# Kernel tuning notes

Measured on AMD Instinct MI355X. Metric: run time of the kernel, lower is better.

The kernel has to match this reference:

```python
import jax, jax.numpy as jnp
import numpy as np

N_EL, N_NB, DIM = 8192, 24, 256
CUTOFF = 5.0
F0, F1 = 32, 16
N_ENV = 8
N_FEAT = 4  # [dist, dx, dy, dz]


def setup_inputs() -> dict:
    key = jax.random.key(0)
    ks = jax.random.split(key, 24)
    d = {}
    d['elec'] = jax.random.normal(ks[0], (N_EL, DIM), jnp.float32)
    d['msg'] = jax.random.normal(ks[1], (N_EL, DIM), jnp.float32)
    # positions inside a box of half the cutoff so pairs are within range
    d['r'] = jax.random.uniform(ks[2], (N_EL, 3), jnp.float32) * (0.5 * CUTOFF)
    d['r_nb'] = jax.random.uniform(ks[3], (N_EL, N_NB, 3), jnp.float32) * (0.5 * CUTOFF)
    d['s'] = jax.random.randint(ks[4], (N_EL,), 0, 2, jnp.int32)
    d['s_nb'] = jax.random.randint(ks[5], (N_EL, N_NB), 0, 2, jnp.int32)
    d['hinit_nb'] = jax.random.normal(ks[6], (N_EL, N_NB, DIM), jnp.float32)
    # parameters
    def lecun(k, shape):
        fan_in = shape[0]
        return jax.random.normal(k, shape, jnp.float32) / np.float32(np.sqrt(fan_in))
    d['W_in'] = lecun(ks[7], (DIM, DIM)); d['b_in'] = jnp.zeros((DIM,), jnp.float32)
    d['ee_scales'] = jax.random.uniform(ks[8], (N_ENV,), jnp.float32, 0.5, CUTOFF)
    d['ee_kernel'] = lecun(ks[9], (N_FEAT, F0))
    d['ee_bias'] = 2.0 * jax.random.normal(ks[10], (F0,), jnp.float32)
    d['Wf'] = lecun(ks[11], (F0 + N_ENV, F1)); d['bf'] = jnp.zeros((F1,), jnp.float32)
    d['Wsame'] = lecun(ks[12], (F1, DIM))
    d['Wdiff'] = lecun(ks[13], (F1, DIM))
    d['W1'] = lecun(ks[14], (DIM, DIM)); d['b1'] = jnp.zeros((DIM,), jnp.float32)
    d['W2'] = lecun(ks[15], (DIM, DIM)); d['b2'] = jnp.zeros((DIM,), jnp.float32)
    d['W3'] = lecun(ks[16], (DIM, DIM)); d['b3'] = jnp.zeros((DIM,), jnp.float32)
    d['scale'] = jnp.float32(1.0)  # FixedScalingFactor (identity at init)
    return d


def _forward(elec, msg, r, r_nb, s, s_nb, hinit_nb,
             W_in, b_in, ee_scales, ee_kernel, ee_bias, Wf, bf,
             Wsame, Wdiff, W1, b1, W2, b2, W3, b3, scale):
    silu = jax.nn.silu
    elec1 = silu(elec @ W_in + b_in)                       # [N, D]
    # get_diff_features: [dist, dx, dy, dz]
    diff = r_nb - r[:, None, :]                             # [N, K, 3]
    dist = jnp.sqrt(jnp.sum(diff * diff, -1) + 1e-12)       # [N, K]
    feats = jnp.concatenate([dist[..., None], diff], -1)    # [N, K, 4]
    spin_mask = s[:, None] == s_nb                          # [N, K]
    # PairwiseFilter: MLP on diff-features + radial envelopes, smooth cutoff
    env = jnp.exp(-jnp.square(dist[..., None] / ee_scales)) # [N, K, E]
    h = silu(feats @ ee_kernel + ee_bias)                   # [N, K, F0]
    h = jnp.concatenate([h, env], -1)                       # [N, K, F0+E]
    x = dist / CUTOFF
    cut = jnp.where(dist < CUTOFF, jnp.square(1.0 - x) * (1.0 + 2.0 * x), 0.0)
    beta = (h @ Wf + bf) * cut[..., None]                   # [N, K, F1]
    gamma = jnp.where(spin_mask[..., None], beta @ Wsame, beta @ Wdiff)  # [N, K, D]
    hinit_msg = jnp.einsum('nid,nid->nd', silu(elec1[:, None] + hinit_nb), gamma)
    out = silu(elec1 @ W1 + b1 + hinit_msg)
    out = silu(out @ W2 + b2 + msg)
    out = silu(out @ W3 + b3)
    return (out + elec1) * scale


def reference(elec, msg, r, r_nb, s, s_nb, hinit_nb,
              W_in, b_in, ee_scales, ee_kernel, ee_bias, Wf, bf,
              Wsame, Wdiff, W1, b1, W2, b2, W3, b3, scale):
    return _forward(elec, msg, r, r_nb, s, s_nb, hinit_nb,
                    W_in, b_in, ee_scales, ee_kernel, ee_bias, Wf, bf,
                    Wsame, Wdiff, W1, b1, W2, b2, W3, b3, scale)
```

## Files before the change

kernel.cpp:

```cpp
#include <hip/hip_runtime.h>

#define DIM 256
#define PDIM 260
#define PD2  264
#define NNB 24
#define NEL 8192
#define ROWS 16
#define NT 512
#define CUTOFF 5.0f

typedef unsigned int u32;
typedef unsigned short u16;
typedef __attribute__((ext_vector_type(8))) short bf16x8;
typedef __attribute__((ext_vector_type(4))) float f32x4;

__device__ __forceinline__ u16 f2b(float f){
  union{float f;u32 i;}v; v.f=f;
  u32 r = v.i + 0x7fffu + ((v.i>>16)&1u);
  return (u16)(r>>16);
}
__device__ __forceinline__ float b2f(u16 u){
  union{u32 i;float f;}v; v.i = ((u32)u)<<16; return v.f;
}
__device__ __forceinline__ float fast_silu(float x){
  float e = __builtin_amdgcn_exp2f(-1.44269504088896340f * x);
  return x * __builtin_amdgcn_rcpf(1.0f + e);
}

__global__ __launch_bounds__(256)
void wprep(const float* __restrict__ W0, const float* __restrict__ W1,
           const float* __restrict__ W2, const float* __restrict__ W3,
           const float* __restrict__ Wsame, const float* __restrict__ Wdiff,
           u16* __restrict__ ws){
  if (blockIdx.x < 1024){
    const int mat = blockIdx.x >> 8;
    const int n   = blockIdx.x & 255;
    const int k   = threadIdx.x;
    const float* W = (mat==0)?W0:(mat==1)?W1:(mat==2)?W2:W3;
    ws[(mat<<16) + (n<<8) + k] = f2b(W[(k<<8) + n]);
  } else {
    const int n = threadIdx.x;
    u16* dst = ws + 4*65536 + n*32;
    #pragma unroll
    for (int kk = 0; kk < 16; kk++){
      dst[kk]    = f2b(Wsame[kk*DIM + n]);
      dst[16+kk] = f2b(Wdiff[kk*DIM + n]);
    }
  }
}

template<int MODE, int ABF16>
__device__ __forceinline__ void gemm_mfma(
    const void* A, u16* sE1b, float* sR1,
    const u16* __restrict__ Wt, const float* __restrict__ bias,
    const float* __restrict__ extraGbl, float* __restrict__ outGbl,
    float scl, int n0, int t)
{
  const int lane = t & 63;
  const int ln   = lane & 15;
  const int quad = lane >> 4;
  const int nt0  = (t >> 6) << 1;
  f32x4 acc0 = {0.f,0.f,0.f,0.f};
  f32x4 acc1 = {0.f,0.f,0.f,0.f};
  const u16* bp0 = Wt + (nt0*16 + ln)*DIM;
  const u16* bp1 = bp0 + 16*DIM;
  #pragma unroll
  for (int ks = 0; ks < 8; ks++){
    const int k0 = ks*32 + quad*8;
    bf16x8 af;
    if (ABF16){
      af = *(const bf16x8*)((const u16*)A + ln*PD2 + k0);
    } else {
      const float* arow = (const float*)A + ln*PDIM;
      float4 a01 = *(const float4*)(arow + k0);
      float4 a23 = *(const float4*)(arow + k0 + 4);
      af[0]=(short)f2b(a01.x); af[1]=(short)f2b(a01.y);
      af[2]=(short)f2b(a01.z); af[3]=(short)f2b(a01.w);
      af[4]=(short)f2b(a23.x); af[5]=(short)f2b(a23.y);
      af[6]=(short)f2b(a23.z); af[7]=(short)f2b(a23.w);
    }
    bf16x8 b0 = *(const bf16x8*)(bp0 + k0);
    bf16x8 b1 = *(const bf16x8*)(bp1 + k0);
    acc0 = __builtin_amdgcn_mfma_f32_16x16x32_bf16(af, b0, acc0, 0, 0, 0);
    acc1 = __builtin_amdgcn_mfma_f32_16x16x32_bf16(af, b1, acc1, 0, 0, 0);
  }
  if (MODE == 2) __syncthreads();
  #pragma unroll
  for (int r = 0; r < 4; r++){
    const int m = quad*4 + r;
    #pragma unroll
    for (int tt = 0; tt < 2; tt++){
      const int n = (nt0+tt)*16 + ln;
      float v = (tt ? acc1[r] : acc0[r]) + bias[n];
      if (MODE == 1) v += sR1[m*PDIM + n];
      if (MODE == 2) v += extraGbl[(size_t)(n0+m)*DIM + n];
      v = fast_silu(v);
      if (MODE == 0)      sE1b[m*PD2 + n] = f2b(v);
      else if (MODE == 3) outGbl[(size_t)(n0+m)*DIM + n] = (v + b2f(sE1b[m*PD2 + n])) * scl;
      else                sR1[m*PDIM + n] = v;
    }
  }
}

__global__ __launch_bounds__(NT, 6)
void fused_moon_kernel(
    const float* __restrict__ elec, const float* __restrict__ msg,
    const float* __restrict__ rpos, const float* __restrict__ rnb,
    const int* __restrict__ s,    const int* __restrict__ snb,
    const float* __restrict__ hinit,
    const float* __restrict__ bin,
    const float* __restrict__ eesc, const float* __restrict__ eek,
    const float* __restrict__ eeb,  const float* __restrict__ Wf,
    const float* __restrict__ bfb,
    const float* __restrict__ b1, const float* __restrict__ b2,
    const float* __restrict__ b3,
    const float* __restrict__ scalep,
    const u16* __restrict__ Wt,
    float* __restrict__ out)
{
  __shared__ float sR1[ROWS*PDIM];
  __shared__ u16   sE1b[ROWS*PD2];
  __shared__ u16   sBC[NNB*16*32];
  const int t  = threadIdx.x;
  const int n0 = blockIdx.x * ROWS;

  {
    const float4* ep = (const float4*)elec;
    #pragma unroll
    for (int h = 0; h < 2; h++){
      const int idx = t + h*NT;
      float4 v = ep[(size_t)n0*64 + idx];
      *(float4*)&sR1[(idx>>6)*PDIM + (idx&63)*4] = v;
    }
  }
  __syncthreads();

  gemm_mfma<0,0>(sR1, sE1b, sR1, Wt, bin, nullptr, nullptr, 0.f, n0, t);

  if (t < ROWS*NNB) {
    const int rr = t / NNB;
    const int k  = t - rr*NNB;
    const int n  = n0 + rr;
    const float* rp  = rpos + n*3;
    const float* rnp = rnb + (n*NNB + k)*3;
    float dx = rnp[0] - rp[0];
    float dy = rnp[1] - rp[1];
    float dz = rnp[2] - rp[2];
    float dist = sqrtf(dx*dx + dy*dy + dz*dz + 1e-12f);
    float feats[4] = {dist, dx, dy, dz};
    float h[32];
    #pragma unroll
    for (int f4 = 0; f4 < 8; f4++){
      float4 a4 = *(const float4*)&eeb[4*f4];
      float av[4] = {a4.x, a4.y, a4.z, a4.w};
      #pragma unroll
      for (int i = 0; i < 4; i++){
        float4 kv = *(const float4*)&eek[i*32 + 4*f4];
        av[0]+=feats[i]*kv.x; av[1]+=feats[i]*kv.y; av[2]+=feats[i]*kv.z; av[3]+=feats[i]*kv.w;
      }
      h[4*f4+0]=fast_silu(av[0]); h[4*f4+1]=fast_silu(av[1]);
      h[4*f4+2]=fast_silu(av[2]); h[4*f4+3]=fast_silu(av[3]);
    }
    float env[8];
    #pragma unroll
    for (int e = 0; e < 8; e++){
      float q = dist * __builtin_amdgcn_rcpf(eesc[e]);
      env[e] = __builtin_amdgcn_exp2f(-1.44269504088896340f * q * q);
    }
    float xx = dist * (1.0f/CUTOFF);
    float cut = (dist < CUTOFF) ? (1.0f-xx)*(1.0f-xx)*(1.0f+2.0f*xx) : 0.0f;
    float barr[16];
    #pragma unroll
    for (int j4 = 0; j4 < 4; j4++){
      float4 a4 = *(const float4*)&bfb[4*j4];
      float av[4] = {a4.x, a4.y, a4.z, a4.w};
      #pragma unroll
      for (int f = 0; f < 40; f++){
        float val = (f < 32) ? h[f] : env[f-32];
        float4 wv = *(const float4*)&Wf[f*16 + 4*j4];
        av[0]+=val*wv.x; av[1]+=val*wv.y; av[2]+=val*wv.z; av[3]+=val*wv.w;
      }
      barr[4*j4+0]=av[0]*cut; barr[4*j4+1]=av[1]*cut;
      barr[4*j4+2]=av[2]*cut; barr[4*j4+3]=av[3]*cut;
    }
    const int m = (s[n] == snb[n*NNB + k]);
    u16 vals[32];
    #pragma unroll
    for (int j = 0; j < 16; j++){
      u16 b = f2b(barr[j]);
      vals[j]    = m ? b : (u16)0;
      vals[16+j] = m ? (u16)0 : b;
    }
    u16* rowp = &sBC[(k*16 + rr)*32];
    #pragma unroll
    for (int c = 0; c < 4; c++){
      const int cp = c ^ ((rr>>1)&3);
      bf16x8 cv;
      #pragma unroll
      for (int j = 0; j < 8; j++) cv[j] = (short)vals[c*8 + j];
      *(bf16x8*)(rowp + cp*8) = cv;
    }
  }
  __syncthreads();

  {
    const int lane = t & 63;
    const int ln   = lane & 15;
    const int quad = lane >> 4;
    const int nt0  = (t >> 6) << 1;
    const u16* Wcat = Wt + 4*65536;
    bf16x8 bs0 = *(const bf16x8*)(Wcat + (nt0*16 + ln)*32 + quad*8);
    bf16x8 bs1 = *(const bf16x8*)(Wcat + ((nt0+1)*16 + ln)*32 + quad*8);
    float e1v[4][2], hm[4][2];
    #pragma unroll
    for (int j = 0; j < 4; j++){
      #pragma unroll
      for (int tt = 0; tt < 2; tt++){
        e1v[j][tt] = b2f(sE1b[(quad*4+j)*PD2 + (nt0+tt)*16 + ln]);
        hm[j][tt] = 0.f;
      }
    }
    const int cswz = (quad ^ ((ln>>1)&3))*8;
    const float* hb = hinit + (size_t)(n0 + quad*4)*NNB*DIM + ln;
    for (int k = 0; k < NNB; k++){
      bf16x8 af = *(const bf16x8*)(&sBC[(k*16 + ln)*32 + cswz]);
      f32x4 z = {0.f,0.f,0.f,0.f};
      f32x4 g0 = __builtin_amdgcn_mfma_f32_16x16x32_bf16(af, bs0, z, 0, 0, 0);
      f32x4 g1 = __builtin_amdgcn_mfma_f32_16x16x32_bf16(af, bs1, z, 0, 0, 0);
      #pragma unroll
      for (int j = 0; j < 4; j++){
        const float* hp = hb + ((size_t)(j*NNB + k))*DIM + nt0*16;
        float h0 = hp[0];
        float h1 = hp[16];
        hm[j][0] += fast_silu(e1v[j][0] + h0) * g0[j];
        hm[j][1] += fast_silu(e1v[j][1] + h1) * g1[j];
      }
    }
    #pragma unroll
    for (int j = 0; j < 4; j++){
      sR1[(quad*4+j)*PDIM + nt0*16 + ln]     = hm[j][0];
      sR1[(quad*4+j)*PDIM + (nt0+1)*16 + ln] = hm[j][1];
    }
  }
  __syncthreads();

  const float scl = scalep[0];

  gemm_mfma<1,1>(sE1b, sE1b, sR1, Wt + (1<<16), b1, nullptr, nullptr, 0.f, n0, t);
  __syncthreads();
  gemm_mfma<2,0>(sR1, sE1b, sR1, Wt + (2<<16), b2, msg, nullptr, 0.f, n0, t);
  __syncthreads();
  gemm_mfma<3,0>(sR1, sE1b, sR1, Wt + (3<<16), b3, nullptr, out, scl, n0, t);
}

extern "C" void kernel_launch(void* const* d_in, const int* in_sizes, int n_in,
                              void* d_out, int out_size, void* d_ws, size_t ws_size,
                              hipStream_t stream) {
  (void)in_sizes; (void)n_in; (void)ws_size; (void)out_size;
  const float* elec  = (const float*)d_in[0];
  const float* msg   = (const float*)d_in[1];
  const float* rpos  = (const float*)d_in[2];
  const float* rnb   = (const float*)d_in[3];
  const int*   s     = (const int*)d_in[4];
  const int*   snb   = (const int*)d_in[5];
  const float* hinit = (const float*)d_in[6];
  const float* Win   = (const float*)d_in[7];
  const float* bin   = (const float*)d_in[8];
  const float* eesc  = (const float*)d_in[9];
  const float* eek   = (const float*)d_in[10];
  const float* eeb   = (const float*)d_in[11];
  const float* Wf    = (const float*)d_in[12];
  const float* bfb   = (const float*)d_in[13];
  const float* Wsame = (const float*)d_in[14];
  const float* Wdiff = (const float*)d_in[15];
  const float* W1    = (const float*)d_in[16];
  const float* b1    = (const float*)d_in[17];
  const float* W2    = (const float*)d_in[18];
  const float* b2    = (const float*)d_in[19];
  const float* W3    = (const float*)d_in[20];
  const float* b3    = (const float*)d_in[21];
  const float* scl   = (const float*)d_in[22];
  float* outp        = (float*)d_out;
  u16*   wt          = (u16*)d_ws;

  wprep<<<dim3(1025), dim3(256), 0, stream>>>(Win, W1, W2, W3, Wsame, Wdiff, wt);
  fused_moon_kernel<<<dim3(NEL/ROWS), dim3(NT), 0, stream>>>(
      elec, msg, rpos, rnb, s, snb, hinit,
      bin, eesc, eek, eeb, Wf, bfb,
      b1, b2, b3, scl, wt, outp);
}
```

Measured before the change: 419.9 us.

## Vectorize hinit neighbor loads via LDS transpose of filter outputs, with prefetch

Each lane now reads four contiguous hinit floats per row with float4 loads, and the next neighbor's values are prefetched in registers. Before, each lane did scalar strided loads. The MFMA filter outputs go through a per-wave LDS buffer so the lane layout matches those loads. The spin-split beta tile is stored at half width with a separate mask array, and the mask is applied when the MFMA operand is built. This adds extra LDS traffic, wave barriers and shared memory, and lowers the launch-bounds occupancy hint from 6 to 4.

Result: faster. 370.5 us (-11.8%).

```diff
diff --git a/kernel.cpp b/kernel.cpp
--- a/kernel.cpp
+++ b/kernel.cpp
@@ -3,6 +3,8 @@
 #define DIM 256
 #define PDIM 260
 #define PD2  264
+#define SBPITCH 20
+#define SGPITCH 40
 #define NNB 24
 #define NEL 8192
 #define ROWS 16
@@ -102,7 +104,7 @@
   }
 }
 
-__global__ __launch_bounds__(NT, 6)
+__global__ __launch_bounds__(NT, 4)
 void fused_moon_kernel(
     const float* __restrict__ elec, const float* __restrict__ msg,
     const float* __restrict__ rpos, const float* __restrict__ rnb,
@@ -120,7 +122,9 @@
 {
   __shared__ float sR1[ROWS*PDIM];
   __shared__ u16   sE1b[ROWS*PD2];
-  __shared__ u16   sBC[NNB*16*32];
+  __shared__ u16   sBC[NNB*16*SBPITCH];
+  __shared__ int   sMask[ROWS*NNB];
+  __shared__ float sG[8*16*SGPITCH];
   const int t  = threadIdx.x;
   const int n0 = blockIdx.x * ROWS;
 
@@ -169,7 +173,7 @@
     }
     float xx = dist * (1.0f/CUTOFF);
     float cut = (dist < CUTOFF) ? (1.0f-xx)*(1.0f-xx)*(1.0f+2.0f*xx) : 0.0f;
-    float barr[16];
+    u16* rowp = &sBC[(k*16 + rr)*SBPITCH];
     #pragma unroll
     for (int j4 = 0; j4 < 4; j4++){
       float4 a4 = *(const float4*)&bfb[4*j4];
@@ -180,26 +184,12 @@
         float4 wv = *(const float4*)&Wf[f*16 + 4*j4];
         av[0]+=val*wv.x; av[1]+=val*wv.y; av[2]+=val*wv.z; av[3]+=val*wv.w;
       }
-      barr[4*j4+0]=av[0]*cut; barr[4*j4+1]=av[1]*cut;
-      barr[4*j4+2]=av[2]*cut; barr[4*j4+3]=av[3]*cut;
-    }
-    const int m = (s[n] == snb[n*NNB + k]);
-    u16 vals[32];
-    #pragma unroll
-    for (int j = 0; j < 16; j++){
-      u16 b = f2b(barr[j]);
-      vals[j]    = m ? b : (u16)0;
-      vals[16+j] = m ? (u16)0 : b;
-    }
-    u16* rowp = &sBC[(k*16 + rr)*32];
-    #pragma unroll
-    for (int c = 0; c < 4; c++){
-      const int cp = c ^ ((rr>>1)&3);
-      bf16x8 cv;
-      #pragma unroll
-      for (int j = 0; j < 8; j++) cv[j] = (short)vals[c*8 + j];
-      *(bf16x8*)(rowp + cp*8) = cv;
-    }
+      ushort4 bv;
+      bv.x = f2b(av[0]*cut); bv.y = f2b(av[1]*cut);
+      bv.z = f2b(av[2]*cut); bv.w = f2b(av[3]*cut);
+      *(ushort4*)(rowp + 4*j4) = bv;
+    }
+    sMask[rr*NNB + k] = (s[n] == snb[n*NNB + k]) ? 1 : 0;
   }
   __syncthreads();
 
@@ -207,40 +197,60 @@
     const int lane = t & 63;
     const int ln   = lane & 15;
     const int quad = lane >> 4;
-    const int nt0  = (t >> 6) << 1;
+    const int w    = t >> 6;
+    const int C0   = w << 5;
     const u16* Wcat = Wt + 4*65536;
-    bf16x8 bs0 = *(const bf16x8*)(Wcat + (nt0*16 + ln)*32 + quad*8);
-    bf16x8 bs1 = *(const bf16x8*)(Wcat + ((nt0+1)*16 + ln)*32 + quad*8);
-    float e1v[4][2], hm[4][2];
-    #pragma unroll
-    for (int j = 0; j < 4; j++){
+    bf16x8 bs0 = *(const bf16x8*)(Wcat + (C0 + ln)*32 + quad*8);
+    bf16x8 bs1 = *(const bf16x8*)(Wcat + (C0 + 16 + ln)*32 + quad*8);
+    float* sGw = &sG[w*16*SGPITCH];
+
+    const int rowA = lane >> 3;
+    const int rowB = rowA + 8;
+    const int c4   = (lane & 7) << 2;
+    float e1A[4], e1B[4];
+    {
+      ushort4 ea = *(const ushort4*)&sE1b[rowA*PD2 + C0 + c4];
+      ushort4 eb = *(const ushort4*)&sE1b[rowB*PD2 + C0 + c4];
+      e1A[0]=b2f(ea.x); e1A[1]=b2f(ea.y); e1A[2]=b2f(ea.z); e1A[3]=b2f(ea.w);
+      e1B[0]=b2f(eb.x); e1B[1]=b2f(eb.y); e1B[2]=b2f(eb.z); e1B[3]=b2f(eb.w);
+    }
+    const float* hpA = hinit + (size_t)(n0 + rowA)*NNB*DIM + C0 + c4;
+    const float* hpB = hpA + (size_t)8*NNB*DIM;
+    float hmA[4] = {0.f,0.f,0.f,0.f};
+    float hmB[4] = {0.f,0.f,0.f,0.f};
+    float4 hA = *(const float4*)(hpA);
+    float4 hB = *(const float4*)(hpB);
+    for (int k = 0; k < NNB; k++){
+      const int kn = (k+1 < NNB) ? (k+1) : (NNB-1);
+      float4 hA2 = *(const float4*)(hpA + kn*DIM);
+      float4 hB2 = *(const float4*)(hpB + kn*DIM);
+      bf16x8 b8 = *(const bf16x8*)(&sBC[(k*16 + ln)*SBPITCH + (quad&1)*8]);
+      const int mm = sMask[ln*NNB + k];
+      const u16 km = (u16)((((quad>>1) ^ mm) != 0) ? 0xFFFFu : 0u);
+      bf16x8 af;
       #pragma unroll
-      for (int tt = 0; tt < 2; tt++){
-        e1v[j][tt] = b2f(sE1b[(quad*4+j)*PD2 + (nt0+tt)*16 + ln]);
-        hm[j][tt] = 0.f;
-      }
-    }
-    const int cswz = (quad ^ ((ln>>1)&3))*8;
-    const float* hb = hinit + (size_t)(n0 + quad*4)*NNB*DIM + ln;
-    for (int k = 0; k < NNB; k++){
-      bf16x8 af = *(const bf16x8*)(&sBC[(k*16 + ln)*32 + cswz]);
+      for (int j = 0; j < 8; j++) af[j] = (short)(((u16)af[j], (u16)b8[j]) & km);
       f32x4 z = {0.f,0.f,0.f,0.f};
       f32x4 g0 = __builtin_amdgcn_mfma_f32_16x16x32_bf16(af, bs0, z, 0, 0, 0);
       f32x4 g1 = __builtin_amdgcn_mfma_f32_16x16x32_bf16(af, bs1, z, 0, 0, 0);
+      __builtin_amdgcn_wave_barrier();
       #pragma unroll
-      for (int j = 0; j < 4; j++){
-        const float* hp = hb + ((size_t)(j*NNB + k))*DIM + nt0*16;
-        float h0 = hp[0];
-        float h1 = hp[16];
-        hm[j][0] += fast_silu(e1v[j][0] + h0) * g0[j];
-        hm[j][1] += fast_silu(e1v[j][1] + h1) * g1[j];
+      for (int r = 0; r < 4; r++){
+        sGw[(quad*4+r)*SGPITCH + ln]      = g0[r];
+        sGw[(quad*4+r)*SGPITCH + 16 + ln] = g1[r];
       }
-    }
-    #pragma unroll
-    for (int j = 0; j < 4; j++){
-      sR1[(quad*4+j)*PDIM + nt0*16 + ln]     = hm[j][0];
-      sR1[(quad*4+j)*PDIM + (nt0+1)*16 + ln] = hm[j][1];
-    }
+      __builtin_amdgcn_wave_barrier();
+      float4 gA = *(const float4*)&sGw[rowA*SGPITCH + c4];
+      float4 gB = *(const float4*)&sGw[rowB*SGPITCH + c4];
+      __builtin_amdgcn_wave_barrier();
+      hmA[0] += fast_silu(e1A[0]+hA.x)*gA.x; hmA[1] += fast_silu(e1A[1]+hA.y)*gA.y;
+      hmA[2] += fast_silu(e1A[2]+hA.z)*gA.z; hmA[3] += fast_silu(e1A[3]+hA.w)*gA.w;
+      hmB[0] += fast_silu(e1B[0]+hB.x)*gB.x; hmB[1] += fast_silu(e1B[1]+hB.y)*gB.y;
+      hmB[2] += fast_silu(e1B[2]+hB.z)*gB.z; hmB[3] += fast_silu(e1B[3]+hB.w)*gB.w;
+      hA = hA2; hB = hB2;
+    }
+    *(float4*)&sR1[rowA*PDIM + C0 + c4] = make_float4(hmA[0],hmA[1],hmA[2],hmA[3]);
+    *(float4*)&sR1[rowB*PDIM + C0 + c4] = make_float4(hmB[0],hmB[1],hmB[2],hmB[3]);
   }
   __syncthreads();
 
```
